# Performance work log

Hardware: AMD Instinct MI355X
Metric: run time of the kernel (lower is better)

## Reference

```python
import jax, jax.numpy as jnp
import numpy as np

STEPS = 100
G = 20.0
N = 250_000  # batch of parallel simulations


def setup_inputs() -> dict:
    key = jax.random.key(0)
    h_initial = jax.random.normal(key, (N,), dtype=jnp.float32) * 10.0
    return {
        "h_initial": h_initial,
        "alpha1": jnp.float32(0.6),
        "alpha2": jnp.float32(0.4),
        "theta": jnp.float32(0.15),
    }


def reference(h_initial, alpha1, alpha2, theta):
    g = jnp.float32(G)
    denom = 1.0 - alpha1 * (1.0 - theta)  # loop-invariant scalar

    def step(h, _):
        y = (g + alpha2 * h) / denom
        yd = y - theta * y
        c = alpha1 * yd + alpha2 * h
        h_new = h + (yd - c)
        return h_new, (y, h_new)

    _, (y_hist, h_hist) = jax.lax.scan(step, h_initial, None, length=STEPS)
    # y_hist, h_hist: [STEPS, N], matching torch.stack over the time loop
    return y_hist, h_hist
```

## Files before the change

kernel.cpp:

```cpp
#include <hip/hip_runtime.h>

#define STEPS 100
#define GCONST 20.0f

typedef float v2f __attribute__((ext_vector_type(2)));

__global__ __launch_bounds__(256) void sim_scan_kernel(
    const float* __restrict__ h0,
    const float* __restrict__ pa1,
    const float* __restrict__ pa2,
    const float* __restrict__ pth,
    float* __restrict__ out,
    int n)
{
    const int nv = n >> 1;
    const int i = blockIdx.x * blockDim.x + threadIdx.x;
    if (i >= nv) return;

    const float a1 = *pa1;
    const float a2 = *pa2;
    const float th = *pth;
    const float denom = 1.0f - a1 * (1.0f - th);

    v2f h = reinterpret_cast<const v2f*>(h0)[i];

    v2f* oy = reinterpret_cast<v2f*>(out) + i;
    v2f* oh = reinterpret_cast<v2f*>(out + (size_t)STEPS * (size_t)n) + i;

    #pragma unroll 5
    for (int t = 0; t < STEPS; ++t) {
        v2f y, yd, c;
        y.x = (GCONST + a2 * h.x) / denom;
        y.y = (GCONST + a2 * h.y) / denom;
        yd.x = y.x - th * y.x;
        yd.y = y.y - th * y.y;
        c.x = a1 * yd.x + a2 * h.x;
        c.y = a1 * yd.y + a2 * h.y;
        h.x = h.x + (yd.x - c.x);
        h.y = h.y + (yd.y - c.y);

        *oy = y;
        *oh = h;
        oy += nv;
        oh += nv;
    }
}

__global__ void sim_scan_tail_kernel(
    const float* __restrict__ h0,
    const float* __restrict__ pa1,
    const float* __restrict__ pa2,
    const float* __restrict__ pth,
    float* __restrict__ out,
    int n, int start)
{
    int i = start + blockIdx.x * blockDim.x + threadIdx.x;
    if (i >= n) return;

    const float a1 = *pa1;
    const float a2 = *pa2;
    const float th = *pth;
    const float denom = 1.0f - a1 * (1.0f - th);

    float h = h0[i];
    float* oy = out + i;
    float* oh = out + (size_t)STEPS * (size_t)n + i;

    for (int t = 0; t < STEPS; ++t) {
        float y = (GCONST + a2 * h) / denom;
        float yd = y - th * y;
        float c = a1 * yd + a2 * h;
        h = h + (yd - c);
        *oy = y;
        *oh = h;
        oy += n;
        oh += n;
    }
}

extern "C" void kernel_launch(void* const* d_in, const int* in_sizes, int n_in,
                              void* d_out, int out_size, void* d_ws, size_t ws_size,
                              hipStream_t stream) {
    const float* h0 = (const float*)d_in[0];
    const float* a1 = (const float*)d_in[1];
    const float* a2 = (const float*)d_in[2];
    const float* th = (const float*)d_in[3];
    float* out = (float*)d_out;

    const int n = in_sizes[0];
    const int nv = n / 2;

    const int block = 256;
    const int grid = (nv + block - 1) / block;
    if (nv > 0) {
        sim_scan_kernel<<<grid, block, 0, stream>>>(h0, a1, a2, th, out, n);
    }
    const int rem_start = nv * 2;
    if (rem_start < n) {
        const int rem = n - rem_start;
        sim_scan_tail_kernel<<<(rem + 63) / 64, 64, 0, stream>>>(
            h0, a1, a2, th, out, n, rem_start);
    }
}
```

Baseline: 200.3 us.

## Split time steps across grid y-dimension with recompute and widen to float4

Each thread now processes four simulations and the 100 time steps are split into 8 chunks along the grid's y-dimension. Each chunk's thread recomputes the recurrence from the start to its first step, then stores only its own slice. This adds parallelism over the time axis (about 8x more threads) so more stores are in flight for this store-bound kernel. The cost is redundant recompute of earlier steps, which includes divides.

Result: slower. 213.7 us (+6.7%).

```diff
diff --git a/kernel.cpp b/kernel.cpp
--- a/kernel.cpp
+++ b/kernel.cpp
@@ -2,8 +2,10 @@
 
 #define STEPS 100
 #define GCONST 20.0f
+#define TSPLIT 8
+#define CHUNK 13
 
-typedef float v2f __attribute__((ext_vector_type(2)));
+typedef float v4f __attribute__((ext_vector_type(4)));
 
 __global__ __launch_bounds__(256) void sim_scan_kernel(
     const float* __restrict__ h0,
@@ -13,31 +15,50 @@
     float* __restrict__ out,
     int n)
 {
-    const int nv = n >> 1;
-    const int i = blockIdx.x * blockDim.x + threadIdx.x;
-    if (i >= nv) return;
+    const int nv = n >> 2;
+    const int j = blockIdx.x * blockDim.x + threadIdx.x;
+    if (j >= nv) return;
+    const int c = blockIdx.y;
+    const int t0 = c * CHUNK;
+    const int t1 = (t0 + CHUNK < STEPS) ? (t0 + CHUNK) : STEPS;
+    if (t0 >= STEPS) return;
 
     const float a1 = *pa1;
     const float a2 = *pa2;
     const float th = *pth;
     const float denom = 1.0f - a1 * (1.0f - th);
 
-    v2f h = reinterpret_cast<const v2f*>(h0)[i];
+    v4f h = reinterpret_cast<const v4f*>(h0)[j];
 
-    v2f* oy = reinterpret_cast<v2f*>(out) + i;
-    v2f* oh = reinterpret_cast<v2f*>(out + (size_t)STEPS * (size_t)n) + i;
-
-    #pragma unroll 5
-    for (int t = 0; t < STEPS; ++t) {
-        v2f y, yd, c;
+    for (int t = 0; t < t0; ++t) {
+        v4f y, yd, cc;
         y.x = (GCONST + a2 * h.x) / denom;
         y.y = (GCONST + a2 * h.y) / denom;
-        yd.x = y.x - th * y.x;
-        yd.y = y.y - th * y.y;
-        c.x = a1 * yd.x + a2 * h.x;
-        c.y = a1 * yd.y + a2 * h.y;
-        h.x = h.x + (yd.x - c.x);
-        h.y = h.y + (yd.y - c.y);
+        y.z = (GCONST + a2 * h.z) / denom;
+        y.w = (GCONST + a2 * h.w) / denom;
+        yd.x = y.x - th * y.x;  yd.y = y.y - th * y.y;
+        yd.z = y.z - th * y.z;  yd.w = y.w - th * y.w;
+        cc.x = a1 * yd.x + a2 * h.x;  cc.y = a1 * yd.y + a2 * h.y;
+        cc.z = a1 * yd.z + a2 * h.z;  cc.w = a1 * yd.w + a2 * h.w;
+        h.x = h.x + (yd.x - cc.x);  h.y = h.y + (yd.y - cc.y);
+        h.z = h.z + (yd.z - cc.z);  h.w = h.w + (yd.w - cc.w);
+    }
+
+    v4f* oy = reinterpret_cast<v4f*>(out) + (size_t)t0 * nv + j;
+    v4f* oh = reinterpret_cast<v4f*>(out + (size_t)STEPS * (size_t)n) + (size_t)t0 * nv + j;
+
+    for (int t = t0; t < t1; ++t) {
+        v4f y, yd, cc;
+        y.x = (GCONST + a2 * h.x) / denom;
+        y.y = (GCONST + a2 * h.y) / denom;
+        y.z = (GCONST + a2 * h.z) / denom;
+        y.w = (GCONST + a2 * h.w) / denom;
+        yd.x = y.x - th * y.x;  yd.y = y.y - th * y.y;
+        yd.z = y.z - th * y.z;  yd.w = y.w - th * y.w;
+        cc.x = a1 * yd.x + a2 * h.x;  cc.y = a1 * yd.y + a2 * h.y;
+        cc.z = a1 * yd.z + a2 * h.z;  cc.w = a1 * yd.w + a2 * h.w;
+        h.x = h.x + (yd.x - cc.x);  h.y = h.y + (yd.y - cc.y);
+        h.z = h.z + (yd.z - cc.z);  h.w = h.w + (yd.w - cc.w);
 
         *oy = y;
         *oh = h;
@@ -88,14 +109,14 @@
     float* out = (float*)d_out;
 
     const int n = in_sizes[0];
-    const int nv = n / 2;
+    const int nv = n / 4;
 
     const int block = 256;
-    const int grid = (nv + block - 1) / block;
+    dim3 grid((nv + block - 1) / block, TSPLIT);
     if (nv > 0) {
         sim_scan_kernel<<<grid, block, 0, stream>>>(h0, a1, a2, th, out, n);
     }
-    const int rem_start = nv * 2;
+    const int rem_start = nv * 4;
     if (rem_start < n) {
         const int rem = n - rem_start;
         sim_scan_tail_kernel<<<(rem + 63) / 64, 64, 0, stream>>>(
```

## Replace sequential scan with closed-form affine solution and flat grid-stride fill

Applied to the files above, without the earlier changes.

Rewrites the per-step recurrence as a closed-form affine map around its fixed point, so each output is h_s + A^t*(h0-h_s) (with y from a matching formula). A tiny single-thread kernel precomputes powers of A into workspace. A grid-stride kernel then writes every output element independently with 16-byte vector stores, which removes the serial dependency and spreads the writes evenly across the grid. The cost is an extra kernel launch, a dependency on the workspace buffer, and float rounding that differs from the step-by-step reference.

Result: no change. 200.9 us (+0.3%).

```diff
diff --git a/kernel.cpp b/kernel.cpp
--- a/kernel.cpp
+++ b/kernel.cpp
@@ -3,9 +3,72 @@
 #define STEPS 100
 #define GCONST 20.0f
 
-typedef float v2f __attribute__((ext_vector_type(2)));
+typedef float v4f __attribute__((ext_vector_type(4)));
 
-__global__ __launch_bounds__(256) void sim_scan_kernel(
+__global__ void build_pow_table(
+    const float* __restrict__ pa1,
+    const float* __restrict__ pa2,
+    const float* __restrict__ pth,
+    float* __restrict__ tbl)
+{
+    if (threadIdx.x == 0 && blockIdx.x == 0) {
+        const float a1 = *pa1, a2 = *pa2, th = *pth;
+        const float denom = 1.0f - a1 * (1.0f - th);
+        const float w = (1.0f - a1) * (1.0f - th);
+        const float A = (1.0f - a2) + w * a2 / denom;
+        float p = 1.0f;
+        for (int t = 0; t <= STEPS; ++t) { tbl[t] = p; p *= A; }
+    }
+}
+
+__global__ __launch_bounds__(256) void sim_fill_kernel(
+    const float* __restrict__ h0,
+    const float* __restrict__ pa1,
+    const float* __restrict__ pa2,
+    const float* __restrict__ pth,
+    const float* __restrict__ tbl,
+    float* __restrict__ out,
+    int n)
+{
+    const unsigned nv = (unsigned)n >> 2;
+    const unsigned half = (unsigned)STEPS * nv;
+    const unsigned total = 2u * half;
+
+    const float a1 = *pa1, a2 = *pa2, th = *pth;
+    const float denom = 1.0f - a1 * (1.0f - th);
+    const float w  = (1.0f - a1) * (1.0f - th);
+    const float A  = (1.0f - a2) + w * a2 / denom;
+    const float B  = w * GCONST / denom;
+    const float hs = B / (1.0f - A);
+    const float ys = (GCONST + a2 * hs) / denom;
+    const float k  = a2 / denom;
+
+    const v4f* __restrict__ h0v = reinterpret_cast<const v4f*>(h0);
+    v4f* __restrict__ out4 = reinterpret_cast<v4f*>(out);
+
+    const unsigned stride = gridDim.x * blockDim.x;
+    for (unsigned g = blockIdx.x * blockDim.x + threadIdx.x; g < total; g += stride) {
+        unsigned gr = g;
+        const bool isH = g >= half;
+        if (isH) gr -= half;
+        const unsigned t  = gr / nv;
+        const unsigned i4 = gr - t * nv;
+
+        const float c1 = isH ? tbl[t + 1] : k * tbl[t];
+        const float c0 = isH ? hs : ys;
+
+        const v4f hv = h0v[i4];
+        v4f val;
+        val.x = c0 + c1 * (hv.x - hs);
+        val.y = c0 + c1 * (hv.y - hs);
+        val.z = c0 + c1 * (hv.z - hs);
+        val.w = c0 + c1 * (hv.w - hs);
+
+        out4[g] = val;
+    }
+}
+
+__global__ void sim_scan_generic_kernel(
     const float* __restrict__ h0,
     const float* __restrict__ pa1,
     const float* __restrict__ pa2,
@@ -13,64 +76,26 @@
     float* __restrict__ out,
     int n)
 {
-    const int nv = n >> 1;
-    const int i = blockIdx.x * blockDim.x + threadIdx.x;
-    if (i >= nv) return;
-
-    const float a1 = *pa1;
-    const float a2 = *pa2;
-    const float th = *pth;
-    const float denom = 1.0f - a1 * (1.0f - th);
-
-    v2f h = reinterpret_cast<const v2f*>(h0)[i];
-
-    v2f* oy = reinterpret_cast<v2f*>(out) + i;
-    v2f* oh = reinterpret_cast<v2f*>(out + (size_t)STEPS * (size_t)n) + i;
-
-    #pragma unroll 5
-    for (int t = 0; t < STEPS; ++t) {
-        v2f y, yd, c;
-        y.x = (GCONST + a2 * h.x) / denom;
-        y.y = (GCONST + a2 * h.y) / denom;
-        yd.x = y.x - th * y.x;
-        yd.y = y.y - th * y.y;
-        c.x = a1 * yd.x + a2 * h.x;
-        c.y = a1 * yd.y + a2 * h.y;
-        h.x = h.x + (yd.x - c.x);
-        h.y = h.y + (yd.y - c.y);
-
-        *oy = y;
-        *oh = h;
-        oy += nv;
-        oh += nv;
-    }
-}
-
-__global__ void sim_scan_tail_kernel(
-    const float* __restrict__ h0,
-    const float* __restrict__ pa1,
-    const float* __restrict__ pa2,
-    const float* __restrict__ pth,
-    float* __restrict__ out,
-    int n, int start)
-{
-    int i = start + blockIdx.x * blockDim.x + threadIdx.x;
+    int i = blockIdx.x * blockDim.x + threadIdx.x;
     if (i >= n) return;
 
-    const float a1 = *pa1;
-    const float a2 = *pa2;
-    const float th = *pth;
+    const float a1 = *pa1, a2 = *pa2, th = *pth;
     const float denom = 1.0f - a1 * (1.0f - th);
+    const float w  = (1.0f - a1) * (1.0f - th);
+    const float A  = (1.0f - a2) + w * a2 / denom;
+    const float B  = w * GCONST / denom;
+    const float hs = B / (1.0f - A);
+    const float ys = (GCONST + a2 * hs) / denom;
+    const float k  = a2 / denom;
 
-    float h = h0[i];
+    float d = h0[i] - hs;
     float* oy = out + i;
     float* oh = out + (size_t)STEPS * (size_t)n + i;
 
     for (int t = 0; t < STEPS; ++t) {
-        float y = (GCONST + a2 * h) / denom;
-        float yd = y - th * y;
-        float c = a1 * yd + a2 * h;
-        h = h + (yd - c);
+        float y = ys + k * d;
+        d *= A;
+        float h = hs + d;
         *oy = y;
         *oh = h;
         oy += n;
@@ -86,19 +111,19 @@
     const float* a2 = (const float*)d_in[2];
     const float* th = (const float*)d_in[3];
     float* out = (float*)d_out;
+    float* tbl = (float*)d_ws;
 
     const int n = in_sizes[0];
-    const int nv = n / 2;
 
-    const int block = 256;
-    const int grid = (nv + block - 1) / block;
-    if (nv > 0) {
-        sim_scan_kernel<<<grid, block, 0, stream>>>(h0, a1, a2, th, out, n);
-    }
-    const int rem_start = nv * 2;
-    if (rem_start < n) {
-        const int rem = n - rem_start;
-        sim_scan_tail_kernel<<<(rem + 63) / 64, 64, 0, stream>>>(
-            h0, a1, a2, th, out, n, rem_start);
+    if ((n & 3) == 0 && n > 0) {
+        build_pow_table<<<1, 64, 0, stream>>>(a1, a2, th, tbl);
+        const unsigned total = (unsigned)(n / 4) * 2u * STEPS;
+        const int block = 256;
+        unsigned blocks = (total + block - 1) / block;
+        if (blocks > 2048u) blocks = 2048u;
+        sim_fill_kernel<<<blocks, block, 0, stream>>>(h0, a1, a2, th, tbl, out, n);
+    } else if (n > 0) {
+        sim_scan_generic_kernel<<<(n + 255) / 256, 256, 0, stream>>>(
+            h0, a1, a2, th, out, n);
     }
 }
```
